# Kernel tuning notes

Measured on AMD Instinct MI355X. Metric: run time of the kernel, lower is better.

The kernel has to match this reference:

```python
import jax, jax.numpy as jnp
import numpy as np

B = 524288
E = 32          # embed_dim
H = 4           # num_heads
D = E // H      # head_dim = 8
NE = 64         # expert_nums
TOP_K = 2
NOISE_EPS = 0.01


def setup_inputs() -> dict:
    key = jax.random.key(0)
    ks = jax.random.split(key, 12)
    inv = 1.0 / np.sqrt(E)
    return {
        "taskID": jax.random.randint(ks[0], (B,), 0, 6),
        "noise": jax.random.normal(ks[1], (B, NE), dtype=jnp.float32),
        "embed_table": jax.random.normal(ks[2], (6, E), dtype=jnp.float32),
        "expert_keys": jax.random.normal(ks[3], (E, E), dtype=jnp.float32),
        "Wq": jax.random.uniform(ks[4], (E, E), minval=-inv, maxval=inv),
        "bq": jnp.zeros((E,), jnp.float32),
        "Wk": jax.random.uniform(ks[5], (E, E), minval=-inv, maxval=inv),
        "bk": jnp.zeros((E,), jnp.float32),
        "Wg": jax.random.uniform(ks[6], (NE, E), minval=-inv, maxval=inv),
        "bg": jax.random.uniform(ks[7], (NE,), minval=-inv, maxval=inv),
        "Wn": jax.random.uniform(ks[8], (NE, E), minval=-inv, maxval=inv),
        "bn": jax.random.uniform(ks[9], (NE,), minval=-inv, maxval=inv),
    }


def reference(taskID, noise, embed_table, expert_keys, Wq, bq, Wk, bk, Wg, bg, Wn, bn):
    b = taskID.shape[0]
    scale = 1.0 / np.sqrt(D)
    # query = task embedding (tgt_len=1); keys = expert_keys, identical across batch
    task_embed = embed_table[taskID]                       # [B, E]
    q = ((task_embed @ Wq.T) + bq) * scale                 # [B, E]
    k = (expert_keys @ Wk.T) + bk                          # [S=E, E] (shared across batch)
    qh = q.reshape(b, H, D)                                # [B, H, D]
    kh = k.reshape(E, H, D)                                # [S, H, D]
    scores = jnp.einsum('bhd,shd->bhs', qh, kh)            # [B, H, S]
    attn = jax.nn.softmax(scores, axis=-1)                 # per-head attn
    attn_weights = attn.mean(axis=1)                       # avg over heads -> [B, S]
    expert_weight = jax.nn.softmax(attn_weights, axis=-1)  # softmax of attn weights
    clean_logits = expert_weight @ Wg.T + bg               # [B, NE]
    noise_std = jax.nn.softplus(expert_weight @ Wn.T + bn) + NOISE_EPS
    logits = clean_logits + noise * noise_std              # train=True path
    k_sel = min(TOP_K + 1, NE)
    top_logits, top_idx = jax.lax.top_k(logits, k_sel)
    top_k_logits = top_logits[:, :TOP_K]
    top_k_idx = top_idx[:, :TOP_K]
    top_k_gates = jax.nn.softmax(top_k_logits, axis=1)
    rows = jnp.arange(b)[:, None]
    gates = jnp.zeros_like(logits).at[rows, top_k_idx].set(top_k_gates)
    load = gates.sum(axis=0)
    return gates, load
```

## Files before the change

kernel.cpp:

```cpp
#include <hip/hip_runtime.h>
#include <hip/hip_bf16.h>
#include <math.h>


#define NE 64
#define NTASK 6
#define GRID_MAIN 1024
#define BLOCK_MAIN 256

__global__ __launch_bounds__(384)
void moe_tables(const float* __restrict__ embed_table,
                const float* __restrict__ expert_keys,
                const float* __restrict__ Wq, const float* __restrict__ bq,
                const float* __restrict__ Wk, const float* __restrict__ bk,
                const float* __restrict__ Wg, const float* __restrict__ bg,
                const float* __restrict__ Wn, const float* __restrict__ bn,
                float* __restrict__ tbl )
{
    __shared__ float s_ek[1024];
    __shared__ float s_wk[1024];
    __shared__ float s_k[1024];
    __shared__ float s_q[NTASK][32];
    __shared__ float s_sc[NTASK][4][32];
    __shared__ float s_ew[NTASK][32];

    const int tid  = threadIdx.x;
    const int wave = tid >> 6;
    const int lane = tid & 63;

    for (int i = tid; i < 1024; i += 384) { s_ek[i] = expert_keys[i]; s_wk[i] = Wk[i]; }
    __syncthreads();

    for (int i = tid; i < 1024; i += 384) {
        int s = i >> 5, e = i & 31;
        float acc = bk[e];
        for (int j = 0; j < 32; ++j) acc += s_ek[s*32 + j] * s_wk[e*32 + j];
        s_k[i] = acc;
    }
    __syncthreads();

    if (lane < 32) {
        float acc = bq[lane];
        for (int j = 0; j < 32; ++j) acc += embed_table[wave*32 + j] * Wq[lane*32 + j];
        s_q[wave][lane] = acc * 0.35355339059327373f;
    }
    __syncthreads();

    for (int r = lane; r < 128; r += 64) {
        int h = r >> 5, s = r & 31;
        float acc = 0.f;
        for (int d = 0; d < 8; ++d) acc += s_q[wave][h*8 + d] * s_k[s*32 + h*8 + d];
        s_sc[wave][h][s] = acc;
    }
    __syncthreads();

    if (lane < 4) {
        int h = lane;
        float m = -1e30f;
        for (int s = 0; s < 32; ++s) m = fmaxf(m, s_sc[wave][h][s]);
        float sum = 0.f;
        for (int s = 0; s < 32; ++s) { float e = expf(s_sc[wave][h][s] - m); s_sc[wave][h][s] = e; sum += e; }
        float inv = 1.f / sum;
        for (int s = 0; s < 32; ++s) s_sc[wave][h][s] *= inv;
    }
    __syncthreads();

    if (lane == 0) {
        float aw[32];
        float m = -1e30f;
        for (int s = 0; s < 32; ++s) {
            float a = 0.25f * (s_sc[wave][0][s] + s_sc[wave][1][s] +
                               s_sc[wave][2][s] + s_sc[wave][3][s]);
            aw[s] = a; m = fmaxf(m, a);
        }
        float sum = 0.f;
        for (int s = 0; s < 32; ++s) { float e = expf(aw[s] - m); aw[s] = e; sum += e; }
        float inv = 1.f / sum;
        for (int s = 0; s < 32; ++s) s_ew[wave][s] = aw[s] * inv;
    }
    __syncthreads();

    {
        int j = lane;
        float c = bg[j], n = bn[j];
        for (int s = 0; s < 32; ++s) {
            float w = s_ew[wave][s];
            c += w * Wg[j*32 + s];
            n += w * Wn[j*32 + s];
        }
        float sp = fmaxf(n, 0.f) + log1pf(expf(-fabsf(n)));
        tbl[(wave*2    )*64 + j] = c;
        tbl[(wave*2 + 1)*64 + j] = sp + 0.01f;
    }
}

__device__ __forceinline__ bool better(float v, int i, float V, int I) {
    return (v > V) || (v == V && i < I);
}

__global__ __launch_bounds__(BLOCK_MAIN)
void moe_gate(const int* __restrict__ taskID,
              const float* __restrict__ noise,
              const float* __restrict__ tbl,
              float* __restrict__ gates,
              float* __restrict__ partials,
              int B)
{
    __shared__ float stbl[NTASK*2*64];
    __shared__ float sload[NE];

    const int tid = threadIdx.x;
    for (int i = tid; i < NTASK*2*64; i += BLOCK_MAIN) stbl[i] = tbl[i];
    if (tid < NE) sload[tid] = 0.f;
    __syncthreads();

    const int wave = tid >> 6;
    const int lane = tid & 63;
    const int grp  = lane >> 4;
    const int gl   = lane & 15;
    const int c0   = gl * 4;

    for (long rb = (long)blockIdx.x * 16; rb < B; rb += (long)gridDim.x * 16) {
        long row = rb + wave*4 + grp;
        if (row < B) {
            int t = taskID[row];
            const float* cl = &stbl[(t*2    )*64];
            const float* ns = &stbl[(t*2 + 1)*64];

            float4 nz = *(const float4*)(noise + row*64 + c0);
            float4 cc = *(const float4*)(cl + c0);
            float4 ss = *(const float4*)(ns + c0);

            float v[4];
            v[0] = cc.x + nz.x * ss.x;
            v[1] = cc.y + nz.y * ss.y;
            v[2] = cc.z + nz.z * ss.z;
            v[3] = cc.w + nz.w * ss.w;

            float v1 = v[0]; int i1 = c0;
            float v2 = -1e30f; int i2 = 1 << 20;
            #pragma unroll
            for (int k = 1; k < 4; ++k) {
                if (v[k] > v1)      { v2 = v1; i2 = i1; v1 = v[k]; i1 = c0 + k; }
                else if (v[k] > v2) { v2 = v[k]; i2 = c0 + k; }
            }

            #pragma unroll
            for (int m = 1; m < 16; m <<= 1) {
                float w1 = __shfl_xor(v1, m); int j1 = __shfl_xor(i1, m);
                float w2 = __shfl_xor(v2, m); int j2 = __shfl_xor(i2, m);
                if (better(w1, j1, v1, i1)) {
                    if (better(v1, i1, w2, j2)) { v2 = v1; i2 = i1; }
                    else                        { v2 = w2; i2 = j2; }
                    v1 = w1; i1 = j1;
                } else if (better(w1, j1, v2, i2)) {
                    v2 = w1; i2 = j1;
                }
            }

            float e2  = expf(v2 - v1);
            float inv = 1.f / (1.f + e2);
            float g1  = inv, g2 = e2 * inv;

            float4 o;
            o.x = (c0     == i1) ? g1 : (c0     == i2) ? g2 : 0.f;
            o.y = (c0 + 1 == i1) ? g1 : (c0 + 1 == i2) ? g2 : 0.f;
            o.z = (c0 + 2 == i1) ? g1 : (c0 + 2 == i2) ? g2 : 0.f;
            o.w = (c0 + 3 == i1) ? g1 : (c0 + 3 == i2) ? g2 : 0.f;
            *(float4*)(gates + row*64 + c0) = o;

            if (gl == 0) {
                atomicAdd(&sload[i1], g1);
                atomicAdd(&sload[i2], g2);
            }
        }
    }
    __syncthreads();
    if (tid < NE) partials[(long)blockIdx.x * NE + tid] = sload[tid];
}

__global__ __launch_bounds__(1024)
void moe_load_reduce(const float* __restrict__ partials, float* __restrict__ load)
{
    __shared__ float s[1024];
    const int tid  = threadIdx.x;
    const int bin  = tid & 63;
    const int part = tid >> 6;
    float acc = 0.f;
    for (int p = part*64; p < part*64 + 64; ++p)
        acc += partials[(long)p * NE + bin];
    s[part*64 + bin] = acc;
    __syncthreads();
    if (tid < NE) {
        float a = 0.f;
        for (int p = 0; p < 16; ++p) a += s[p*64 + tid];
        load[tid] = a;
    }
}

extern "C" void kernel_launch(void* const* d_in, const int* in_sizes, int n_in,
                              void* d_out, int out_size, void* d_ws, size_t ws_size,
                              hipStream_t stream)
{
    const int*   taskID      = (const int*)  d_in[0];
    const float* noise       = (const float*)d_in[1];
    const float* embed_table = (const float*)d_in[2];
    const float* expert_keys = (const float*)d_in[3];
    const float* Wq          = (const float*)d_in[4];
    const float* bq          = (const float*)d_in[5];
    const float* Wk          = (const float*)d_in[6];
    const float* bk          = (const float*)d_in[7];
    const float* Wg          = (const float*)d_in[8];
    const float* bg          = (const float*)d_in[9];
    const float* Wn          = (const float*)d_in[10];
    const float* bn          = (const float*)d_in[11];

    const int B = in_sizes[0];

    float* gates = (float*)d_out;
    float* load  = gates + (size_t)B * NE;

    float* tbl      = (float*)d_ws;
    float* partials = (float*)((char*)d_ws + 4096);

    moe_tables<<<1, 384, 0, stream>>>(embed_table, expert_keys,
                                      Wq, bq, Wk, bk, Wg, bg, Wn, bn, tbl);
    moe_gate<<<GRID_MAIN, BLOCK_MAIN, 0, stream>>>(taskID, noise, tbl,
                                                   gates, partials, B);
    moe_load_reduce<<<1, 1024, 0, stream>>>(partials, load);
}
```

Before: 285.1 us.

## Rework gate kernel: 8 lanes per row, packed 64-bit top-2 keys, nontemporal stores

The gate kernel now gives each row to 8 lanes holding 8 columns each instead of 16 lanes holding 4, and it doubles the grid. Top-2 selection packs value and index into a sortable 64-bit key, so the shuffle merge is a max/min network rather than branchy comparisons. Gate outputs are written with nontemporal stores to avoid polluting the cache. The kernel takes an occupancy hint, and the load reduction is parameterized by grid size. The cost is 64-bit shuffles and more partial sums to reduce.

```diff
diff --git a/kernel.cpp b/kernel.cpp
--- a/kernel.cpp
+++ b/kernel.cpp
@@ -5,8 +5,10 @@
 
 #define NE 64
 #define NTASK 6
-#define GRID_MAIN 1024
+#define GRID_MAIN 2048
 #define BLOCK_MAIN 256
+
+typedef float f32x4 __attribute__((ext_vector_type(4)));
 
 __global__ __launch_bounds__(384)
 void moe_tables(const float* __restrict__ embed_table,
@@ -94,11 +96,20 @@
     }
 }
 
-__device__ __forceinline__ bool better(float v, int i, float V, int I) {
-    return (v > V) || (v == V && i < I);
-}
-
-__global__ __launch_bounds__(BLOCK_MAIN)
+__device__ __forceinline__ unsigned long long mkkey(float f, int idx) {
+    unsigned u  = __float_as_uint(f);
+    unsigned su = (u & 0x80000000u) ? ~u : (u | 0x80000000u);
+    return ((unsigned long long)su << 32) | (unsigned)(63 - idx);
+}
+__device__ __forceinline__ float keyval(unsigned long long k) {
+    unsigned su = (unsigned)(k >> 32);
+    unsigned u  = (su & 0x80000000u) ? (su ^ 0x80000000u) : ~su;
+    return __uint_as_float(u);
+}
+__device__ __forceinline__ unsigned long long umax64(unsigned long long a, unsigned long long b) { return a > b ? a : b; }
+__device__ __forceinline__ unsigned long long umin64(unsigned long long a, unsigned long long b) { return a < b ? a : b; }
+
+__global__ __launch_bounds__(BLOCK_MAIN, 8)
 void moe_gate(const int* __restrict__ taskID,
               const float* __restrict__ noise,
               const float* __restrict__ tbl,
@@ -106,73 +117,82 @@
               float* __restrict__ partials,
               int B)
 {
-    __shared__ float stbl[NTASK*2*64];
+    __shared__ float stbl[NTASK*128];
     __shared__ float sload[NE];
 
     const int tid = threadIdx.x;
-    for (int i = tid; i < NTASK*2*64; i += BLOCK_MAIN) stbl[i] = tbl[i];
+    for (int i = tid; i < NTASK*128; i += BLOCK_MAIN) stbl[i] = tbl[i];
     if (tid < NE) sload[tid] = 0.f;
     __syncthreads();
 
-    const int wave = tid >> 6;
-    const int lane = tid & 63;
-    const int grp  = lane >> 4;
-    const int gl   = lane & 15;
-    const int c0   = gl * 4;
-
-    for (long rb = (long)blockIdx.x * 16; rb < B; rb += (long)gridDim.x * 16) {
-        long row = rb + wave*4 + grp;
-        if (row < B) {
-            int t = taskID[row];
-            const float* cl = &stbl[(t*2    )*64];
-            const float* ns = &stbl[(t*2 + 1)*64];
-
-            float4 nz = *(const float4*)(noise + row*64 + c0);
-            float4 cc = *(const float4*)(cl + c0);
-            float4 ss = *(const float4*)(ns + c0);
-
-            float v[4];
-            v[0] = cc.x + nz.x * ss.x;
-            v[1] = cc.y + nz.y * ss.y;
-            v[2] = cc.z + nz.z * ss.z;
-            v[3] = cc.w + nz.w * ss.w;
-
-            float v1 = v[0]; int i1 = c0;
-            float v2 = -1e30f; int i2 = 1 << 20;
-            #pragma unroll
-            for (int k = 1; k < 4; ++k) {
-                if (v[k] > v1)      { v2 = v1; i2 = i1; v1 = v[k]; i1 = c0 + k; }
-                else if (v[k] > v2) { v2 = v[k]; i2 = c0 + k; }
-            }
-
-            #pragma unroll
-            for (int m = 1; m < 16; m <<= 1) {
-                float w1 = __shfl_xor(v1, m); int j1 = __shfl_xor(i1, m);
-                float w2 = __shfl_xor(v2, m); int j2 = __shfl_xor(i2, m);
-                if (better(w1, j1, v1, i1)) {
-                    if (better(v1, i1, w2, j2)) { v2 = v1; i2 = i1; }
-                    else                        { v2 = w2; i2 = j2; }
-                    v1 = w1; i1 = j1;
-                } else if (better(w1, j1, v2, i2)) {
-                    v2 = w1; i2 = j1;
-                }
-            }
-
-            float e2  = expf(v2 - v1);
-            float inv = 1.f / (1.f + e2);
-            float g1  = inv, g2 = e2 * inv;
-
-            float4 o;
-            o.x = (c0     == i1) ? g1 : (c0     == i2) ? g2 : 0.f;
-            o.y = (c0 + 1 == i1) ? g1 : (c0 + 1 == i2) ? g2 : 0.f;
-            o.z = (c0 + 2 == i1) ? g1 : (c0 + 2 == i2) ? g2 : 0.f;
-            o.w = (c0 + 3 == i1) ? g1 : (c0 + 3 == i2) ? g2 : 0.f;
-            *(float4*)(gates + row*64 + c0) = o;
-
-            if (gl == 0) {
-                atomicAdd(&sload[i1], g1);
-                atomicAdd(&sload[i2], g2);
-            }
+    const int sub = tid >> 3;
+    const int gl  = tid & 7;
+    const int c0  = gl * 8;
+
+    const long stride = (long)gridDim.x * 32;
+    for (long row = (long)blockIdx.x * 32 + sub; row < B; row += stride) {
+        const int t = taskID[row];
+        const float* cl = &stbl[t * 128];
+
+        const float4* np = (const float4*)(noise + row * 64 + c0);
+        float4 nz0 = np[0];
+        float4 nz1 = np[1];
+        float4 cc0 = *(const float4*)(cl + c0);
+        float4 cc1 = *(const float4*)(cl + c0 + 4);
+        float4 ss0 = *(const float4*)(cl + 64 + c0);
+        float4 ss1 = *(const float4*)(cl + 64 + c0 + 4);
+
+        float v[8];
+        v[0] = fmaf(nz0.x, ss0.x, cc0.x);
+        v[1] = fmaf(nz0.y, ss0.y, cc0.y);
+        v[2] = fmaf(nz0.z, ss0.z, cc0.z);
+        v[3] = fmaf(nz0.w, ss0.w, cc0.w);
+        v[4] = fmaf(nz1.x, ss1.x, cc1.x);
+        v[5] = fmaf(nz1.y, ss1.y, cc1.y);
+        v[6] = fmaf(nz1.z, ss1.z, cc1.z);
+        v[7] = fmaf(nz1.w, ss1.w, cc1.w);
+
+        unsigned long long k1 = mkkey(v[0], c0), k2 = 0ull;
+        #pragma unroll
+        for (int j = 1; j < 8; ++j) {
+            unsigned long long k = mkkey(v[j], c0 + j);
+            if (k > k1)      { k2 = k1; k1 = k; }
+            else if (k > k2) { k2 = k; }
+        }
+
+        #pragma unroll
+        for (int m = 1; m < 8; m <<= 1) {
+            unsigned long long p1 = __shfl_xor((unsigned long long)k1, m);
+            unsigned long long p2 = __shfl_xor((unsigned long long)k2, m);
+            unsigned long long hi = umax64(k1, p1);
+            unsigned long long lo = umin64(k1, p1);
+            k2 = umax64(lo, umax64(k2, p2));
+            k1 = hi;
+        }
+
+        const int i1 = 63 - (int)(k1 & 63u);
+        const int i2 = 63 - (int)(k2 & 63u);
+        const float v1 = keyval(k1);
+        const float v2 = keyval(k2);
+
+        const float e   = expf(v2 - v1);
+        const float inv = 1.f / (1.f + e);
+        const float g1  = inv, g2 = e * inv;
+
+        float o[8];
+        #pragma unroll
+        for (int j = 0; j < 8; ++j) {
+            const int col = c0 + j;
+            o[j] = (col == i1) ? g1 : ((col == i2) ? g2 : 0.f);
+        }
+        f32x4 o0 = { o[0], o[1], o[2], o[3] };
+        f32x4 o1 = { o[4], o[5], o[6], o[7] };
+        __builtin_nontemporal_store(o0, (f32x4*)(gates + row * 64 + c0));
+        __builtin_nontemporal_store(o1, (f32x4*)(gates + row * 64 + c0 + 4));
+
+        if (gl == 0) {
+            atomicAdd(&sload[i1], g1);
+            atomicAdd(&sload[i2], g2);
         }
     }
     __syncthreads();
@@ -180,20 +200,22 @@
 }
 
 __global__ __launch_bounds__(1024)
-void moe_load_reduce(const float* __restrict__ partials, float* __restrict__ load)
+void moe_load_reduce(const float* __restrict__ partials,
+                     float* __restrict__ load, int nparts)
 {
     __shared__ float s[1024];
     const int tid  = threadIdx.x;
     const int bin  = tid & 63;
     const int part = tid >> 6;
+    const int per  = nparts >> 4;
     float acc = 0.f;
-    for (int p = part*64; p < part*64 + 64; ++p)
+    for (int p = part * per; p < (part + 1) * per; ++p)
         acc += partials[(long)p * NE + bin];
-    s[part*64 + bin] = acc;
+    s[part * 64 + bin] = acc;
     __syncthreads();
     if (tid < NE) {
         float a = 0.f;
-        for (int p = 0; p < 16; ++p) a += s[p*64 + tid];
+        for (int p = 0; p < 16; ++p) a += s[p * 64 + tid];
         load[tid] = a;
     }
 }
@@ -227,5 +249,5 @@
                                       Wq, bq, Wk, bk, Wg, bg, Wn, bn, tbl);
     moe_gate<<<GRID_MAIN, BLOCK_MAIN, 0, stream>>>(taskID, noise, tbl,
                                                    gates, partials, B);
-    moe_load_reduce<<<1, 1024, 0, stream>>>(partials, load);
-}
+    moe_load_reduce<<<1, 1024, 0, stream>>>(partials, load, GRID_MAIN);
+}
```

After: 312.5 us. +9.6%, slower.
